# Performance work log

Hardware: AMD Instinct MI355X
Metric: run time of the kernel (lower is better)

The kernel has to match this reference:

```python
import jax, jax.numpy as jnp
import numpy as np

N, K = 16384, 16          # nodes, neighbors per node
IN, HID, OUT = 256, 512, 512
HEADS, A = 8, 64          # heads * attention_size = 512
EPS = 1e-5


def _layernorm(x, g, b):
    m = x.mean(-1, keepdims=True)
    v = x.var(-1, keepdims=True)
    return (x - m) / jnp.sqrt(v + EPS) * g + b


def setup_inputs() -> dict:
    key = jax.random.key(0)
    ks = jax.random.split(key, 16)
    def lin(k, i, o):
        kw, kb = jax.random.split(k)
        w = jax.random.normal(kw, (i, o), jnp.float32) / np.sqrt(i).astype(np.float32)
        b = jax.random.normal(kb, (o,), jnp.float32) * 0.01
        return w, b
    inp = {}
    inp["data"] = jax.random.normal(ks[0], (N, IN), jnp.float32)
    inp["neighbors"] = jax.random.randint(ks[1], (N, K), 0, N, jnp.int32)
    inp["mlp_w0"], inp["mlp_b0"] = lin(ks[2], IN, HID)
    inp["mlp_w1"], inp["mlp_b1"] = lin(ks[3], HID, HID)
    inp["mlp_w2"], inp["mlp_b2"] = lin(ks[4], HID, HID)
    inp["pd_w"], inp["pd_b"] = lin(ks[5], IN, HID)   # project_down
    inp["pi_w"], inp["pi_b"] = lin(ks[6], IN, OUT)   # project_in
    inp["q_w"], inp["q_b"] = lin(ks[7], HID, HEADS * A)
    inp["k_w"], inp["k_b"] = lin(ks[8], HID, HEADS * A)
    inp["v_w"], inp["v_b"] = lin(ks[9], HID, HEADS * A)
    inp["o_w"], inp["o_b"] = lin(ks[10], HEADS * A, OUT)
    inp["ln1_g"] = jnp.ones((HID,), jnp.float32)
    inp["ln1_b"] = jnp.zeros((HID,), jnp.float32)
    inp["ln2_g"] = jnp.ones((OUT,), jnp.float32)
    inp["ln2_b"] = jnp.zeros((OUT,), jnp.float32)
    return inp


def reference(data, neighbors, mlp_w0, mlp_b0, mlp_w1, mlp_b1, mlp_w2, mlp_b2,
              pd_w, pd_b, pi_w, pi_b, q_w, q_b, k_w, k_b, v_w, v_b, o_w, o_b,
              ln1_g, ln1_b, ln2_g, ln2_b):
    # --- local MLP branch (3-layer MLP, elu between layers) ---
    h = jax.nn.elu(data @ mlp_w0 + mlp_b0)
    h = jax.nn.elu(h @ mlp_w1 + mlp_b1)
    h = h @ mlp_w2 + mlp_b2
    pd = data @ pd_w + pd_b                 # project_down(data), reused twice
    local = h + pd                          # MLP(data) + project_down(data)
    # dropout is identity in eval mode
    local = jax.nn.elu(_layernorm(local + pd, ln1_g, ln1_b))
    # --- neighbour dot multi-head attention ---
    q = (local @ q_w + q_b).reshape(N, HEADS, A)
    kk = (local @ k_w + k_b)
    vv = (local @ v_w + v_b)
    kn = kk[neighbors].reshape(N, K, HEADS, A)   # irregular gather
    vn = vv[neighbors].reshape(N, K, HEADS, A)
    scores = jnp.einsum('nha,nkha->nhk', q, kn) / np.float32(np.sqrt(A))
    w = jax.nn.softmax(scores, axis=-1)
    attn = jnp.einsum('nhk,nkha->nha', w, vn).reshape(N, HEADS * A)
    interaction = attn @ o_w + o_b
    # --- residual + output norm ---
    return _layernorm(interaction + data @ pi_w + pi_b, ln2_g, ln2_b)
```

## Files before the change

kernel.cpp:

```cpp
#include <hip/hip_runtime.h>

typedef _Float16 h16;
typedef _Float16 h16x8 __attribute__((ext_vector_type(8)));
typedef _Float16 h16x4 __attribute__((ext_vector_type(4)));
typedef float f32x4 __attribute__((ext_vector_type(4)));

#define DEV static __device__ __forceinline__

static constexpr size_t OFF_DATA = 0;
static constexpr size_t OFF_W0T  = 4194304;
static constexpr size_t OFF_W1T  = 4325376;
static constexpr size_t OFF_W2PD = 4587520;
static constexpr size_t OFF_QKVT = 4980736;
static constexpr size_t OFF_OPIT = 5767168;
static constexpr size_t OFF_X1   = 6160384;
static constexpr size_t OFF_X2   = 14548992;
static constexpr size_t OFF_KV   = OFF_X1;
static constexpr size_t OFF_P    = 22937600;

DEV void gload16(const void* g, void* l)
{
    __builtin_amdgcn_global_load_lds(
        (__attribute__((address_space(1))) void*)(void*)g,
        (__attribute__((address_space(3))) void*)l, 16, 0, 0);
}

DEV float eluf(float x) { return x > 0.f ? x : __expf(x) - 1.f; }

__global__ __launch_bounds__(256)
void k_cvt_data(const float* __restrict__ src, h16* __restrict__ dst)
{
    size_t i = ((size_t)blockIdx.x * 256 + threadIdx.x) * 4;
    float4 v = *(const float4*)(src + i);
    h16x4 o;
    o[0] = (h16)v.x; o[1] = (h16)v.y; o[2] = (h16)v.z; o[3] = (h16)v.w;
    *(h16x4*)(dst + i) = o;
}

__global__ void k_prep_w(const float* __restrict__ w0, const float* __restrict__ w1,
                         const float* __restrict__ w2, const float* __restrict__ pdw,
                         const float* __restrict__ qw, const float* __restrict__ kw,
                         const float* __restrict__ vw, const float* __restrict__ ow,
                         const float* __restrict__ piw, h16* __restrict__ ws)
{
    int b = blockIdx.x;
    const float* src; h16* dst; int K, dstStride, dstKOff = 0, tb; float scale = 1.f;
    const int N = 512;
    if (b < 128)       { src = w0;  dst = ws + OFF_W0T;           K = 256; dstStride = 256; tb = 0; }
    else if (b < 384)  { src = w1;  dst = ws + OFF_W1T;           K = 512; dstStride = 512; tb = 128; }
    else if (b < 640)  { src = w2;  dst = ws + OFF_W2PD;          K = 512; dstStride = 768; tb = 384; }
    else if (b < 768)  { src = pdw; dst = ws + OFF_W2PD;          K = 256; dstStride = 768; dstKOff = 512; scale = 2.f; tb = 640; }
    else if (b < 1024) { src = qw;  dst = ws + OFF_QKVT;          K = 512; dstStride = 512; tb = 768; }
    else if (b < 1280) { src = kw;  dst = ws + OFF_QKVT + 262144; K = 512; dstStride = 512; tb = 1024; }
    else if (b < 1536) { src = vw;  dst = ws + OFF_QKVT + 524288; K = 512; dstStride = 512; tb = 1280; }
    else if (b < 1792) { src = ow;  dst = ws + OFF_OPIT;          K = 512; dstStride = 768; tb = 1536; }
    else               { src = piw; dst = ws + OFF_OPIT;          K = 256; dstStride = 768; dstKOff = 512; tb = 1792; }
    int t = b - tb;
    int tilesK = K >> 5;
    int tk = t % tilesK, tn = t / tilesK;
    __shared__ float tile[32][33];
    int tx = threadIdx.x, ty = threadIdx.y;
    #pragma unroll
    for (int r = 0; r < 32; r += 8)
        tile[ty + r][tx] = src[(size_t)(tk * 32 + ty + r) * N + tn * 32 + tx] * scale;
    __syncthreads();
    #pragma unroll
    for (int r = 0; r < 32; r += 8) {
        int n = tn * 32 + ty + r, k = tk * 32 + tx;
        dst[(size_t)n * dstStride + dstKOff + k] = (h16)tile[tx][ty + r];
    }
}

template<int BIASMODE, bool DOELU>
__global__ __launch_bounds__(256)
void k_gemm(const h16* __restrict__ A1, const h16* __restrict__ A2,
            const int K1, const int K2,
            const h16* __restrict__ BT,
            const float* __restrict__ bias1, const float* __restrict__ bias2,
            const float* __restrict__ bias3, const float b2scale,
            h16* __restrict__ out, h16* __restrict__ out2, const int N)
{
    const int Kt = K1 + K2;
    __shared__ __align__(16) h16 sA[128 * 32];
    __shared__ __align__(16) h16 sB[128 * 32];
    const int tid  = threadIdx.x;
    const int lane = tid & 63;
    const int mBase = blockIdx.y * 128, nBase = blockIdx.x * 128;
    const int wm = ((tid >> 7) & 1) * 64;
    const int wn = ((tid >> 6) & 1) * 64;
    const f32x4 zero = {0.f, 0.f, 0.f, 0.f};
    f32x4 acc[4][4];
    #pragma unroll
    for (int i = 0; i < 4; ++i) {
        #pragma unroll
        for (int j = 0; j < 4; ++j) acc[i][j] = zero;
    }

    const int ldR = tid >> 2;
    const int ldC = (tid & 3) * 8;
    const int lm = lane & 15, lk = (lane >> 4) * 8;

    for (int k0 = 0; k0 < Kt; k0 += 32) {
        const h16* Ab; int Ak, As;
        if (k0 < K1) { Ab = A1; Ak = k0;      As = K1; }
        else         { Ab = A2; Ak = k0 - K1; As = K2; }
        #pragma unroll
        for (int r = 0; r < 2; ++r) {
            const int row = r * 64 + ldR;
            gload16(Ab + (size_t)(mBase + row) * As + Ak + ldC, &sA[row * 32 + ldC]);
            gload16(BT + (size_t)(nBase + row) * Kt + k0 + ldC, &sB[row * 32 + ldC]);
        }
        __syncthreads();
        h16x8 af[4], bfr[4];
        #pragma unroll
        for (int i = 0; i < 4; ++i) af[i]  = *(const h16x8*)&sA[(wm + i * 16 + lm) * 32 + lk];
        #pragma unroll
        for (int j = 0; j < 4; ++j) bfr[j] = *(const h16x8*)&sB[(wn + j * 16 + lm) * 32 + lk];
        #pragma unroll
        for (int i = 0; i < 4; ++i) {
            #pragma unroll
            for (int j = 0; j < 4; ++j)
                acc[i][j] = __builtin_amdgcn_mfma_f32_16x16x32_f16(af[i], bfr[j], acc[i][j], 0, 0, 0);
        }
        __syncthreads();
    }

    const int lr4 = (lane >> 4) * 4;
    #pragma unroll
    for (int j = 0; j < 4; ++j) {
        const int col = nBase + wn + j * 16 + lm;
        float bv;
        if (BIASMODE == 0) bv = bias1[col];
        else if (BIASMODE == 1) bv = bias1[col] + b2scale * bias2[col];
        else {
            const int seg = col >> 9;
            const float* bp = seg == 0 ? bias1 : (seg == 1 ? bias2 : bias3);
            bv = bp[col & 511];
        }
        #pragma unroll
        for (int i = 0; i < 4; ++i) {
            const int row0 = mBase + wm + i * 16 + lr4;
            #pragma unroll
            for (int r = 0; r < 4; ++r) {
                float v = acc[i][j][r] + bv;
                if (DOELU) v = eluf(v);
                if (BIASMODE == 2) {
                    if (col < 512) out [(size_t)(row0 + r) * 512  + col]         = (h16)v;
                    else           out2[(size_t)(row0 + r) * 1024 + (col - 512)] = (h16)v;
                } else {
                    out[(size_t)(row0 + r) * N + col] = (h16)v;
                }
            }
        }
    }
}

template<bool DOELU, bool OUTF32>
__global__ __launch_bounds__(256)
void k_ln(const h16* __restrict__ X, const float* __restrict__ g, const float* __restrict__ b,
          h16* __restrict__ outH, float* __restrict__ outF)
{
    const int row  = blockIdx.x * 4 + (threadIdx.x >> 6);
    const int lane = threadIdx.x & 63;
    const h16x8 xv = *(const h16x8*)(X + (size_t)row * 512 + lane * 8);
    float v[8], s = 0.f, ss = 0.f;
    #pragma unroll
    for (int k = 0; k < 8; ++k) { v[k] = (float)xv[k]; s += v[k]; ss += v[k] * v[k]; }
    #pragma unroll
    for (int m = 1; m < 64; m <<= 1) { s += __shfl_xor(s, m, 64); ss += __shfl_xor(ss, m, 64); }
    const float mean = s * (1.f / 512.f);
    const float var  = ss * (1.f / 512.f) - mean * mean;
    const float rstd = rsqrtf(var + 1e-5f);
    #pragma unroll
    for (int k = 0; k < 8; ++k) {
        const int c = lane * 8 + k;
        float y = (v[k] - mean) * rstd * g[c] + b[c];
        if (DOELU) y = eluf(y);
        if (OUTF32) outF[(size_t)row * 512 + c] = y;
        else        outH[(size_t)row * 512 + c] = (h16)y;
    }
}

__global__ __launch_bounds__(256)
void k_attn(const h16* __restrict__ Q, const h16* __restrict__ KV,
            const int* __restrict__ nbr, h16* __restrict__ outA)
{
    const int n = blockIdx.x;
    __shared__ __align__(16) h16 sQ[512];
    __shared__ __align__(16) h16 sK[16][520];
    __shared__ __align__(16) h16 sV[16][520];
    __shared__ float sW[8][16];
    __shared__ int sNb[16];
    const int tid = threadIdx.x, lane = tid & 63, wave = tid >> 6;
    if (tid < 16) sNb[tid] = nbr[n * 16 + tid];
    __syncthreads();
    if (wave == 0)
        *(h16x8*)&sQ[lane * 8] = *(const h16x8*)&Q[(size_t)n * 512 + lane * 8];
    #pragma unroll
    for (int r = 0; r < 8; ++r) {
        const int p = wave * 8 + r;
        const int arr = p >> 4, j = p & 15;
        const h16x8 val = *(const h16x8*)&KV[(size_t)sNb[j] * 1024 + arr * 512 + lane * 8];
        h16* dstp = arr ? &sV[j][lane * 8] : &sK[j][lane * 8];
        *(h16x8*)dstp = val;
    }
    __syncthreads();
    if (tid < 128) {
        const int h = tid >> 4, j = tid & 15;
        const h16x8* qv = (const h16x8*)&sQ[h * 64];
        const h16x8* kv = (const h16x8*)&sK[j][h * 64];
        float s = 0.f;
        #pragma unroll
        for (int c = 0; c < 8; ++c) {
            h16x8 qa = qv[c], ka = kv[c];
            #pragma unroll
            for (int e = 0; e < 8; ++e) s += (float)qa[e] * (float)ka[e];
        }
        s *= 0.125f;
        float mx = s;
        #pragma unroll
        for (int m = 1; m < 16; m <<= 1) mx = fmaxf(mx, __shfl_xor(mx, m, 64));
        const float e = __expf(s - mx);
        float sum = e;
        #pragma unroll
        for (int m = 1; m < 16; m <<= 1) sum += __shfl_xor(sum, m, 64);
        sW[h][j] = e / sum;
    }
    __syncthreads();
    #pragma unroll
    for (int t = 0; t < 2; ++t) {
        const int o = tid + t * 256;
        const int h = o >> 6, a = o & 63;
        float acc = 0.f;
        #pragma unroll
        for (int j = 0; j < 16; ++j) acc += sW[h][j] * (float)sV[j][h * 64 + a];
        outA[(size_t)n * 512 + o] = (h16)acc;
    }
}

extern "C" void kernel_launch(void* const* d_in, const int* in_sizes, int n_in,
                              void* d_out, int out_size, void* d_ws, size_t ws_size,
                              hipStream_t stream)
{
    const float* data = (const float*)d_in[0];
    const int*   nbr  = (const int*)d_in[1];
    const float* w0   = (const float*)d_in[2];
    const float* b0   = (const float*)d_in[3];
    const float* w1   = (const float*)d_in[4];
    const float* b1   = (const float*)d_in[5];
    const float* w2   = (const float*)d_in[6];
    const float* b2   = (const float*)d_in[7];
    const float* pdw  = (const float*)d_in[8];
    const float* pdb  = (const float*)d_in[9];
    const float* piw  = (const float*)d_in[10];
    const float* pib  = (const float*)d_in[11];
    const float* qw   = (const float*)d_in[12];
    const float* qb   = (const float*)d_in[13];
    const float* kw   = (const float*)d_in[14];
    const float* kb   = (const float*)d_in[15];
    const float* vw   = (const float*)d_in[16];
    const float* vb   = (const float*)d_in[17];
    const float* ow   = (const float*)d_in[18];
    const float* ob   = (const float*)d_in[19];
    const float* ln1g = (const float*)d_in[20];
    const float* ln1b = (const float*)d_in[21];
    const float* ln2g = (const float*)d_in[22];
    const float* ln2b = (const float*)d_in[23];
    h16*   ws  = (h16*)d_ws;
    float* out = (float*)d_out;
    h16*   qbuf = (h16*)d_out;

    k_cvt_data<<<4096, 256, 0, stream>>>(data, ws + OFF_DATA);
    k_prep_w<<<1920, dim3(32, 8), 0, stream>>>(w0, w1, w2, pdw, qw, kw, vw, ow, piw, ws);

    dim3 gA(4, 128);
    dim3 gQ(12, 128);
    k_gemm<0, true ><<<gA, 256, 0, stream>>>(ws + OFF_DATA, nullptr, 256, 0, ws + OFF_W0T,
                                             b0, nullptr, nullptr, 0.f,
                                             ws + OFF_X1, nullptr, 512);
    k_gemm<0, true ><<<gA, 256, 0, stream>>>(ws + OFF_X1, nullptr, 512, 0, ws + OFF_W1T,
                                             b1, nullptr, nullptr, 0.f,
                                             ws + OFF_X2, nullptr, 512);
    k_gemm<1, false><<<gA, 256, 0, stream>>>(ws + OFF_X2, ws + OFF_DATA, 512, 256, ws + OFF_W2PD,
                                             b2, pdb, nullptr, 2.f,
                                             ws + OFF_P, nullptr, 512);
    k_ln<true, false><<<4096, 256, 0, stream>>>(ws + OFF_P, ln1g, ln1b, ws + OFF_P, nullptr);
    k_gemm<2, false><<<gQ, 256, 0, stream>>>(ws + OFF_P, nullptr, 512, 0, ws + OFF_QKVT,
                                             qb, kb, vb, 0.f,
                                             qbuf, ws + OFF_KV, 1536);
    k_attn<<<16384, 256, 0, stream>>>(qbuf, ws + OFF_KV, nbr, ws + OFF_P);
    k_gemm<1, false><<<gA, 256, 0, stream>>>(ws + OFF_P, ws + OFF_DATA, 512, 256, ws + OFF_OPIT,
                                             ob, pib, nullptr, 1.f,
                                             ws + OFF_X1, nullptr, 512);
    k_ln<false, true><<<4096, 256, 0, stream>>>(ws + OFF_X1, ln2g, ln2b, nullptr, out);
}
```

Before: 346.7 us.

## Use 8-wave GEMM tiles and register-resident attention with wave-split K/V

The GEMM kernel moves from 4 to 8 waves per 128x128 tile. Each wave now computes a 64x32 sub-tile, and each thread issues one async LDS load per operand instead of two. The attention kernel no longer stages gathered K/V rows in shared memory. Each wave keeps 8 neighbour rows in registers, computes partial Q·K dot products with shuffle reductions, and accumulates weighted V partials that are summed through a small shared buffer. The intent is more latency hiding and less LDS traffic and sync, at the cost of extra shuffles and fewer MFMAs per wave.

```diff
diff --git a/kernel.cpp b/kernel.cpp
--- a/kernel.cpp
+++ b/kernel.cpp
@@ -3,6 +3,7 @@
 typedef _Float16 h16;
 typedef _Float16 h16x8 __attribute__((ext_vector_type(8)));
 typedef _Float16 h16x4 __attribute__((ext_vector_type(4)));
+typedef _Float16 h16x2 __attribute__((ext_vector_type(2)));
 typedef float f32x4 __attribute__((ext_vector_type(4)));
 
 #define DEV static __device__ __forceinline__
@@ -72,7 +73,7 @@
 }
 
 template<int BIASMODE, bool DOELU>
-__global__ __launch_bounds__(256)
+__global__ __launch_bounds__(512, 4)
 void k_gemm(const h16* __restrict__ A1, const h16* __restrict__ A2,
             const int K1, const int K2,
             const h16* __restrict__ BT,
@@ -86,14 +87,15 @@
     const int tid  = threadIdx.x;
     const int lane = tid & 63;
     const int mBase = blockIdx.y * 128, nBase = blockIdx.x * 128;
-    const int wm = ((tid >> 7) & 1) * 64;
-    const int wn = ((tid >> 6) & 1) * 64;
+    const int w  = tid >> 6;
+    const int wm = (w >> 2) * 64;
+    const int wn = (w & 3) * 32;
     const f32x4 zero = {0.f, 0.f, 0.f, 0.f};
-    f32x4 acc[4][4];
+    f32x4 acc[4][2];
     #pragma unroll
     for (int i = 0; i < 4; ++i) {
         #pragma unroll
-        for (int j = 0; j < 4; ++j) acc[i][j] = zero;
+        for (int j = 0; j < 2; ++j) acc[i][j] = zero;
     }
 
     const int ldR = tid >> 2;
@@ -104,22 +106,18 @@
         const h16* Ab; int Ak, As;
         if (k0 < K1) { Ab = A1; Ak = k0;      As = K1; }
         else         { Ab = A2; Ak = k0 - K1; As = K2; }
-        #pragma unroll
-        for (int r = 0; r < 2; ++r) {
-            const int row = r * 64 + ldR;
-            gload16(Ab + (size_t)(mBase + row) * As + Ak + ldC, &sA[row * 32 + ldC]);
-            gload16(BT + (size_t)(nBase + row) * Kt + k0 + ldC, &sB[row * 32 + ldC]);
-        }
+        gload16(Ab + (size_t)(mBase + ldR) * As + Ak + ldC, &sA[ldR * 32 + ldC]);
+        gload16(BT + (size_t)(nBase + ldR) * Kt + k0 + ldC, &sB[ldR * 32 + ldC]);
         __syncthreads();
-        h16x8 af[4], bfr[4];
+        h16x8 af[4], bfr[2];
         #pragma unroll
         for (int i = 0; i < 4; ++i) af[i]  = *(const h16x8*)&sA[(wm + i * 16 + lm) * 32 + lk];
         #pragma unroll
-        for (int j = 0; j < 4; ++j) bfr[j] = *(const h16x8*)&sB[(wn + j * 16 + lm) * 32 + lk];
+        for (int j = 0; j < 2; ++j) bfr[j] = *(const h16x8*)&sB[(wn + j * 16 + lm) * 32 + lk];
         #pragma unroll
         for (int i = 0; i < 4; ++i) {
             #pragma unroll
-            for (int j = 0; j < 4; ++j)
+            for (int j = 0; j < 2; ++j)
                 acc[i][j] = __builtin_amdgcn_mfma_f32_16x16x32_f16(af[i], bfr[j], acc[i][j], 0, 0, 0);
         }
         __syncthreads();
@@ -127,7 +125,7 @@
 
     const int lr4 = (lane >> 4) * 4;
     #pragma unroll
-    for (int j = 0; j < 4; ++j) {
+    for (int j = 0; j < 2; ++j) {
         const int col = nBase + wn + j * 16 + lm;
         float bv;
         if (BIASMODE == 0) bv = bias1[col];
@@ -186,37 +184,47 @@
             const int* __restrict__ nbr, h16* __restrict__ outA)
 {
     const int n = blockIdx.x;
-    __shared__ __align__(16) h16 sQ[512];
-    __shared__ __align__(16) h16 sK[16][520];
-    __shared__ __align__(16) h16 sV[16][520];
+    const int tid = threadIdx.x, lane = tid & 63, wave = tid >> 6;
+    __shared__ float sS[8][16];
     __shared__ float sW[8][16];
-    __shared__ int sNb[16];
-    const int tid = threadIdx.x, lane = tid & 63, wave = tid >> 6;
-    if (tid < 16) sNb[tid] = nbr[n * 16 + tid];
+    __shared__ __align__(16) float sP[2][512];
+    const int h = lane >> 3;
+    const int cbase = lane * 8;
+    const int isV = wave >> 1;
+    const int jbase = (wave & 1) * 8;
+
+    h16x8 rows[8];
+    #pragma unroll
+    for (int r = 0; r < 8; ++r) {
+        const int j = nbr[n * 16 + jbase + r];
+        rows[r] = *(const h16x8*)&KV[(size_t)j * 1024 + (size_t)isV * 512 + cbase];
+    }
+
+    if (!isV) {
+        const h16x8 qv = *(const h16x8*)&Q[(size_t)n * 512 + cbase];
+        float part[8];
+        #pragma unroll
+        for (int r = 0; r < 8; ++r) {
+            float s = 0.f;
+            #pragma unroll
+            for (int e = 0; e < 8; ++e) s += (float)qv[e] * (float)rows[r][e];
+            part[r] = s;
+        }
+        #pragma unroll
+        for (int m = 1; m < 8; m <<= 1) {
+            #pragma unroll
+            for (int r = 0; r < 8; ++r) part[r] += __shfl_xor(part[r], m, 64);
+        }
+        if ((lane & 7) == 0) {
+            #pragma unroll
+            for (int r = 0; r < 8; ++r) sS[h][jbase + r] = part[r] * 0.125f;
+        }
+    }
     __syncthreads();
-    if (wave == 0)
-        *(h16x8*)&sQ[lane * 8] = *(const h16x8*)&Q[(size_t)n * 512 + lane * 8];
-    #pragma unroll
-    for (int r = 0; r < 8; ++r) {
-        const int p = wave * 8 + r;
-        const int arr = p >> 4, j = p & 15;
-        const h16x8 val = *(const h16x8*)&KV[(size_t)sNb[j] * 1024 + arr * 512 + lane * 8];
-        h16* dstp = arr ? &sV[j][lane * 8] : &sK[j][lane * 8];
-        *(h16x8*)dstp = val;
-    }
-    __syncthreads();
+
     if (tid < 128) {
-        const int h = tid >> 4, j = tid & 15;
-        const h16x8* qv = (const h16x8*)&sQ[h * 64];
-        const h16x8* kv = (const h16x8*)&sK[j][h * 64];
-        float s = 0.f;
-        #pragma unroll
-        for (int c = 0; c < 8; ++c) {
-            h16x8 qa = qv[c], ka = kv[c];
-            #pragma unroll
-            for (int e = 0; e < 8; ++e) s += (float)qa[e] * (float)ka[e];
-        }
-        s *= 0.125f;
+        const int hh = tid >> 4, j = tid & 15;
+        float s = sS[hh][j];
         float mx = s;
         #pragma unroll
         for (int m = 1; m < 16; m <<= 1) mx = fmaxf(mx, __shfl_xor(mx, m, 64));
@@ -224,18 +232,31 @@
         float sum = e;
         #pragma unroll
         for (int m = 1; m < 16; m <<= 1) sum += __shfl_xor(sum, m, 64);
-        sW[h][j] = e / sum;
+        sW[hh][j] = e / sum;
     }
     __syncthreads();
-    #pragma unroll
-    for (int t = 0; t < 2; ++t) {
-        const int o = tid + t * 256;
-        const int h = o >> 6, a = o & 63;
-        float acc = 0.f;
-        #pragma unroll
-        for (int j = 0; j < 16; ++j) acc += sW[h][j] * (float)sV[j][h * 64 + a];
-        outA[(size_t)n * 512 + o] = (h16)acc;
-    }
+
+    if (isV) {
+        float acc[8];
+        #pragma unroll
+        for (int e = 0; e < 8; ++e) acc[e] = 0.f;
+        #pragma unroll
+        for (int r = 0; r < 8; ++r) {
+            const float wj = sW[h][jbase + r];
+            #pragma unroll
+            for (int e = 0; e < 8; ++e) acc[e] += wj * (float)rows[r][e];
+        }
+        float* dst = &sP[wave & 1][cbase];
+        *(f32x4*)dst       = *(const f32x4*)&acc[0];
+        *(f32x4*)(dst + 4) = *(const f32x4*)&acc[4];
+    }
+    __syncthreads();
+
+    const int c = tid * 2;
+    const float v0 = sP[0][c] + sP[1][c];
+    const float v1 = sP[0][c + 1] + sP[1][c + 1];
+    h16x2 o; o[0] = (h16)v0; o[1] = (h16)v1;
+    *(h16x2*)&outA[(size_t)n * 512 + c] = o;
 }
 
 extern "C" void kernel_launch(void* const* d_in, const int* in_sizes, int n_in,
@@ -275,21 +296,21 @@
 
     dim3 gA(4, 128);
     dim3 gQ(12, 128);
-    k_gemm<0, true ><<<gA, 256, 0, stream>>>(ws + OFF_DATA, nullptr, 256, 0, ws + OFF_W0T,
+    k_gemm<0, true ><<<gA, 512, 0, stream>>>(ws + OFF_DATA, nullptr, 256, 0, ws + OFF_W0T,
                                              b0, nullptr, nullptr, 0.f,
                                              ws + OFF_X1, nullptr, 512);
-    k_gemm<0, true ><<<gA, 256, 0, stream>>>(ws + OFF_X1, nullptr, 512, 0, ws + OFF_W1T,
+    k_gemm<0, true ><<<gA, 512, 0, stream>>>(ws + OFF_X1, nullptr, 512, 0, ws + OFF_W1T,
                                              b1, nullptr, nullptr, 0.f,
                                              ws + OFF_X2, nullptr, 512);
-    k_gemm<1, false><<<gA, 256, 0, stream>>>(ws + OFF_X2, ws + OFF_DATA, 512, 256, ws + OFF_W2PD,
+    k_gemm<1, false><<<gA, 512, 0, stream>>>(ws + OFF_X2, ws + OFF_DATA, 512, 256, ws + OFF_W2PD,
                                              b2, pdb, nullptr, 2.f,
                                              ws + OFF_P, nullptr, 512);
     k_ln<true, false><<<4096, 256, 0, stream>>>(ws + OFF_P, ln1g, ln1b, ws + OFF_P, nullptr);
-    k_gemm<2, false><<<gQ, 256, 0, stream>>>(ws + OFF_P, nullptr, 512, 0, ws + OFF_QKVT,
+    k_gemm<2, false><<<gQ, 512, 0, stream>>>(ws + OFF_P, nullptr, 512, 0, ws + OFF_QKVT,
                                              qb, kb, vb, 0.f,
                                              qbuf, ws + OFF_KV, 1536);
     k_attn<<<16384, 256, 0, stream>>>(qbuf, ws + OFF_KV, nbr, ws + OFF_P);
-    k_gemm<1, false><<<gA, 256, 0, stream>>>(ws + OFF_P, ws + OFF_DATA, 512, 256, ws + OFF_OPIT,
+    k_gemm<1, false><<<gA, 512, 0, stream>>>(ws + OFF_P, ws + OFF_DATA, 512, 256, ws + OFF_OPIT,
                                              ob, pib, nullptr, 1.f,
                                              ws + OFF_X1, nullptr, 512);
     k_ln<false, true><<<4096, 256, 0, stream>>>(ws + OFF_X1, ln2g, ln2b, nullptr, out);
```

New measurement: 331.1 us. -4.5%, faster.
